# Kernel optimization log

Hardware: AMD Instinct MI355X
Metric: run time of the kernel (lower is better)

## Reference

```python
import jax, jax.numpy as jnp
import numpy as np

B, S, D = 8, 2048, 512

def setup_inputs() -> dict:
    key = jax.random.key(0)
    k1, k2, k3 = jax.random.split(key, 3)
    context = jax.random.normal(k1, (B, S, D), dtype=jnp.float32)
    # nn.Linear default init ~ U(-1/sqrt(D), 1/sqrt(D)); scale keeps softmax sane
    bound = 1.0 / np.sqrt(D)
    W_in = jax.random.uniform(k2, (D, D), dtype=jnp.float32, minval=-bound, maxval=bound)
    W_out = jax.random.uniform(k3, (D, D), dtype=jnp.float32, minval=-bound, maxval=bound)
    return {"context": context, "W_in": W_in, "W_out": W_out}

def reference(context, W_in, W_out):
    # linear_in: x @ W_in.T (torch Linear convention)
    c = jnp.einsum('bsd,ed->bse', context, W_in)            # [B,S,D]
    scores = jnp.einsum('bsd,btd->bst', c, c)               # [B,S,S], no 1/sqrt(d) scale
    attn = jax.nn.softmax(scores, axis=-1)                  # [B,S,S]
    ctx = jnp.einsum('bst,btd->bsd', attn, c)               # [B,S,D]
    out = jnp.einsum('bsd,ed->bse', jnp.tanh(ctx), W_out)   # linear_out
    return out, attn
```

## Files before the change

### kernel.cpp

```cpp
#include <hip/hip_runtime.h>
#include <cstdint>
#include <cstddef>

#define Bc 8
#define Sc 2048
#define Dc 512

typedef float f32x4 __attribute__((ext_vector_type(4)));
typedef __bf16 bf16x8 __attribute__((ext_vector_type(8)));

__device__ __forceinline__ void gload_lds16(const void* g, void* l) {
    __builtin_amdgcn_global_load_lds((const __attribute__((address_space(1))) void*)g,
                                     (__attribute__((address_space(3))) void*)l, 16, 0, 0);
}

__device__ __forceinline__ f32x4 mfma16x16x32(bf16x8 a, bf16x8 b, f32x4 c) {
    return __builtin_amdgcn_mfma_f32_16x16x32_bf16(a, b, c, 0, 0, 0);
}

__global__ void k_convert_w(const float* __restrict__ wi, const float* __restrict__ wo,
                            __bf16* __restrict__ wib, __bf16* __restrict__ wob) {
    int i = blockIdx.x * 256 + threadIdx.x;
    wib[i] = (__bf16)wi[i];
    wob[i] = (__bf16)wo[i];
}

template <bool STATS>
__global__ __launch_bounds__(256) void k_gemm_bf16(
        const __bf16* __restrict__ A, const __bf16* __restrict__ Bt,
        float* __restrict__ C, float2* __restrict__ stats,
        int lda, int ldb, int ldc, int K,
        size_t aOffZ, size_t bOffZ, size_t cOffZ)
{
    __shared__ alignas(16) __bf16 smem[2 * 128 * 64];
    __bf16* As = smem;
    __bf16* Bs = smem + 128 * 64;
    const int tid  = threadIdx.x;
    const int wave = tid >> 6, lane = tid & 63;
    const int waveM = wave >> 1, waveN = wave & 1;
    const int row0 = blockIdx.y * 128;
    const int col0 = blockIdx.x * 128;
    A  += (size_t)blockIdx.z * aOffZ;
    Bt += (size_t)blockIdx.z * bOffZ;
    C  += (size_t)blockIdx.z * cOffZ;

    f32x4 acc[4][4] = {};

    for (int k0 = 0; k0 < K; k0 += 64) {
        #pragma unroll
        for (int i = 0; i < 4; ++i) {
            int flat = i * 2048 + wave * 512 + lane * 8;
            int r  = flat >> 6;
            int cc = (flat >> 3) & 7;
            int gc = (cc ^ (r & 7)) << 3;
            gload_lds16(A  + (size_t)(row0 + r) * lda + k0 + gc, As + i * 2048 + wave * 512);
            gload_lds16(Bt + (size_t)(col0 + r) * ldb + k0 + gc, Bs + i * 2048 + wave * 512);
        }
        __syncthreads();
        #pragma unroll
        for (int ks = 0; ks < 2; ++ks) {
            const int kc = ks * 4 + (lane >> 4);
            bf16x8 av[4], bv[4];
            #pragma unroll
            for (int mi = 0; mi < 4; ++mi) {
                int r = waveM * 64 + mi * 16 + (lane & 15);
                av[mi] = *(const bf16x8*)&As[r * 64 + ((kc ^ (r & 7)) << 3)];
            }
            #pragma unroll
            for (int ni = 0; ni < 4; ++ni) {
                int r = waveN * 64 + ni * 16 + (lane & 15);
                bv[ni] = *(const bf16x8*)&Bs[r * 64 + ((kc ^ (r & 7)) << 3)];
            }
            #pragma unroll
            for (int mi = 0; mi < 4; ++mi)
                #pragma unroll
                for (int ni = 0; ni < 4; ++ni)
                    acc[mi][ni] = mfma16x16x32(av[mi], bv[ni], acc[mi][ni]);
        }
        __syncthreads();
    }

    const int rb = (lane >> 4) << 2;
    const int cb = lane & 15;
    #pragma unroll
    for (int mi = 0; mi < 4; ++mi)
        #pragma unroll
        for (int ni = 0; ni < 4; ++ni) {
            int gr = row0 + waveM * 64 + mi * 16 + rb;
            int gc = col0 + waveN * 64 + ni * 16 + cb;
            #pragma unroll
            for (int rr = 0; rr < 4; ++rr)
                C[(size_t)(gr + rr) * ldc + gc] = acc[mi][ni][rr];
        }

    if constexpr (STATS) {
        float2* sm = (float2*)smem;
        #pragma unroll
        for (int mi = 0; mi < 4; ++mi)
            #pragma unroll
            for (int rr = 0; rr < 4; ++rr) {
                float mx = fmaxf(fmaxf(acc[mi][0][rr], acc[mi][1][rr]),
                                 fmaxf(acc[mi][2][rr], acc[mi][3][rr]));
                #pragma unroll
                for (int off = 1; off < 16; off <<= 1) mx = fmaxf(mx, __shfl_xor(mx, off));
                float zs = 0.f;
                #pragma unroll
                for (int ni = 0; ni < 4; ++ni) zs += __expf(acc[mi][ni][rr] - mx);
                #pragma unroll
                for (int off = 1; off < 16; off <<= 1) zs += __shfl_xor(zs, off);
                if ((lane & 15) == 0)
                    sm[waveN * 128 + waveM * 64 + mi * 16 + rb + rr] = make_float2(mx, zs);
            }
        __syncthreads();
        if (tid < 128) {
            float2 a2 = sm[tid], b2 = sm[128 + tid];
            float M = fmaxf(a2.x, b2.x);
            float Z = a2.y * __expf(a2.x - M) + b2.y * __expf(b2.x - M);
            stats[((size_t)blockIdx.z * Sc + row0 + tid) * 16 + blockIdx.x] = make_float2(M, Z);
        }
    }
}

__global__ __launch_bounds__(256) void k_stat_combine(const float2* __restrict__ stats,
                                                      float2* __restrict__ rowstat) {
    int r = blockIdx.x * 256 + threadIdx.x;
    float2 s[16];
    #pragma unroll
    for (int i = 0; i < 16; ++i) s[i] = stats[(size_t)r * 16 + i];
    float M = s[0].x;
    #pragma unroll
    for (int i = 1; i < 16; ++i) M = fmaxf(M, s[i].x);
    float Z = 0.f;
    #pragma unroll
    for (int i = 0; i < 16; ++i) Z += s[i].y * __expf(s[i].x - M);
    rowstat[r] = make_float2(M, 1.f / Z);
}

__global__ __launch_bounds__(512) void k_pv_fused(
        float* __restrict__ attn,
        const __bf16* __restrict__ cT,
        const float2* __restrict__ rowstat,
        __bf16* __restrict__ ctx)
{
    __shared__ alignas(16) __bf16 As[64 * 64];
    __shared__ alignas(16) __bf16 Bs[512 * 64];
    const int tid  = threadIdx.x;
    const int wave = tid >> 6, lane = tid & 63;
    const int b    = blockIdx.y;
    const int row0 = blockIdx.x * 64;
    float* sc = attn + (size_t)b * Sc * Sc;
    const __bf16* Bt = cT + (size_t)b * Dc * Sc;

    const int ar = tid >> 3;
    const int ac = (tid & 7) * 8;
    const float2 st = rowstat[b * Sc + row0 + ar];
    const float m_row = st.x, zinv = st.y;
    const int c8a  = ac >> 3;
    const int aoff = ar * 64 + ((c8a ^ (ar & 7)) << 3);

    f32x4 acc[4][4] = {};

    f32x4 s0 = *(const f32x4*)&sc[(size_t)(row0 + ar) * Sc + ac];
    f32x4 s1 = *(const f32x4*)&sc[(size_t)(row0 + ar) * Sc + ac + 4];

    for (int kt = 0; kt < Sc; kt += 64) {
        #pragma unroll
        for (int i = 0; i < 8; ++i) {
            int chunk = i * 512 + wave * 64 + lane;
            int r  = chunk >> 3;
            int cc = chunk & 7;
            gload_lds16(Bt + (size_t)r * Sc + kt + ((cc ^ (r & 7)) << 3),
                        Bs + (size_t)(i * 512 + wave * 64) * 8);
        }
        f32x4 p0, p1;
        #pragma unroll
        for (int j = 0; j < 4; ++j) {
            p0[j] = __expf(s0[j] - m_row) * zinv;
            p1[j] = __expf(s1[j] - m_row) * zinv;
        }
        *(f32x4*)&sc[(size_t)(row0 + ar) * Sc + kt + ac]     = p0;
        *(f32x4*)&sc[(size_t)(row0 + ar) * Sc + kt + ac + 4] = p1;
        bf16x8 pb;
        #pragma unroll
        for (int j = 0; j < 4; ++j) { pb[j] = (__bf16)p0[j]; pb[4 + j] = (__bf16)p1[j]; }
        *(bf16x8*)&As[aoff] = pb;
        __syncthreads();
        if (kt + 64 < Sc) {
            s0 = *(const f32x4*)&sc[(size_t)(row0 + ar) * Sc + kt + 64 + ac];
            s1 = *(const f32x4*)&sc[(size_t)(row0 + ar) * Sc + kt + 64 + ac + 4];
        }
        #pragma unroll
        for (int ks = 0; ks < 2; ++ks) {
            const int kc = ks * 4 + (lane >> 4);
            bf16x8 av[4], bv[4];
            #pragma unroll
            for (int mi = 0; mi < 4; ++mi) {
                int r = mi * 16 + (lane & 15);
                av[mi] = *(const bf16x8*)&As[r * 64 + ((kc ^ (r & 7)) << 3)];
            }
            #pragma unroll
            for (int ni = 0; ni < 4; ++ni) {
                int r = wave * 64 + ni * 16 + (lane & 15);
                bv[ni] = *(const bf16x8*)&Bs[r * 64 + ((kc ^ (r & 7)) << 3)];
            }
            #pragma unroll
            for (int mi = 0; mi < 4; ++mi)
                #pragma unroll
                for (int ni = 0; ni < 4; ++ni)
                    acc[mi][ni] = mfma16x16x32(av[mi], bv[ni], acc[mi][ni]);
        }
        __syncthreads();
    }

    const int rb = (lane >> 4) << 2;
    const int cb = lane & 15;
    #pragma unroll
    for (int mi = 0; mi < 4; ++mi)
        #pragma unroll
        for (int ni = 0; ni < 4; ++ni) {
            int gr = row0 + mi * 16 + rb;
            int gc = wave * 64 + ni * 16 + cb;
            #pragma unroll
            for (int rr = 0; rr < 4; ++rr)
                ctx[(size_t)(b * Sc + gr + rr) * Dc + gc] = (__bf16)tanhf(acc[mi][ni][rr]);
        }
}

__global__ __launch_bounds__(256) void k_cproj(
        const float* __restrict__ A, const __bf16* __restrict__ Bt,
        __bf16* __restrict__ Cb, __bf16* __restrict__ CTb)
{
    __shared__ alignas(16) char smem[49152];
    float*  Asf = (float*)smem;
    __bf16* Bs  = (__bf16*)(smem + 32768);
    const int tid  = threadIdx.x;
    const int wave = tid >> 6, lane = tid & 63;
    const int waveM = wave >> 1, waveN = wave & 1;
    const int row0 = blockIdx.y * 128;
    const int col0 = blockIdx.x * 128;

    f32x4 acc[4][4] = {};

    for (int k0 = 0; k0 < Dc; k0 += 64) {
        #pragma unroll
        for (int i = 0; i < 8; ++i) {
            int flat = i * 1024 + wave * 256 + lane * 4;
            int r  = flat >> 6;
            int cc = (flat >> 2) & 15;
            int gc = (cc ^ (r & 15)) << 2;
            gload_lds16(A + (size_t)(row0 + r) * Dc + k0 + gc, Asf + i * 1024 + wave * 256);
        }
        #pragma unroll
        for (int i = 0; i < 4; ++i) {
            int flat = i * 2048 + wave * 512 + lane * 8;
            int r  = flat >> 6;
            int cc = (flat >> 3) & 7;
            int gc = (cc ^ (r & 7)) << 3;
            gload_lds16(Bt + (size_t)(col0 + r) * Dc + k0 + gc, Bs + i * 2048 + wave * 512);
        }
        __syncthreads();
        #pragma unroll
        for (int ks = 0; ks < 2; ++ks) {
            const int kc8 = ks * 4 + (lane >> 4);
            const int kc4 = kc8 << 1;
            bf16x8 av[4], bv[4];
            #pragma unroll
            for (int mi = 0; mi < 4; ++mi) {
                int r  = waveM * 64 + mi * 16 + (lane & 15);
                int r4 = r & 15;
                f32x4 lo = *(const f32x4*)&Asf[r * 64 + (((kc4    ) ^ r4) << 2)];
                f32x4 hi = *(const f32x4*)&Asf[r * 64 + (((kc4 + 1) ^ r4) << 2)];
                bf16x8 a;
                a[0] = (__bf16)lo[0]; a[1] = (__bf16)lo[1]; a[2] = (__bf16)lo[2]; a[3] = (__bf16)lo[3];
                a[4] = (__bf16)hi[0]; a[5] = (__bf16)hi[1]; a[6] = (__bf16)hi[2]; a[7] = (__bf16)hi[3];
                av[mi] = a;
            }
            #pragma unroll
            for (int ni = 0; ni < 4; ++ni) {
                int r = waveN * 64 + ni * 16 + (lane & 15);
                bv[ni] = *(const bf16x8*)&Bs[r * 64 + ((kc8 ^ (r & 7)) << 3)];
            }
            #pragma unroll
            for (int mi = 0; mi < 4; ++mi)
                #pragma unroll
                for (int ni = 0; ni < 4; ++ni)
                    acc[mi][ni] = mfma16x16x32(av[mi], bv[ni], acc[mi][ni]);
        }
        __syncthreads();
    }

    const int rb = (lane >> 4) << 2;
    const int cb = lane & 15;
    __bf16* T = (__bf16*)smem;
    #pragma unroll
    for (int mi = 0; mi < 4; ++mi)
        #pragma unroll
        for (int ni = 0; ni < 4; ++ni) {
            int lr = waveM * 64 + mi * 16 + rb;
            int lc = waveN * 64 + ni * 16 + cb;
            #pragma unroll
            for (int rr = 0; rr < 4; ++rr) {
                __bf16 h = (__bf16)acc[mi][ni][rr];
                Cb[(size_t)(row0 + lr + rr) * Dc + col0 + lc] = h;
                T[lc * 136 + lr + rr] = h;
            }
        }
    __syncthreads();
    const int bb = row0 >> 11;
    const int s0 = row0 & 2047;
    #pragma unroll
    for (int i = 0; i < 8; ++i) {
        int n  = i * 16 + (tid >> 4);
        int mo = (tid & 15) * 8;
        bf16x8 v = *(const bf16x8*)&T[n * 136 + mo];
        *(bf16x8*)&CTb[(size_t)bb * Dc * Sc + (size_t)(col0 + n) * Sc + s0 + mo] = v;
    }
}

extern "C" void kernel_launch(void* const* d_in, const int* in_sizes, int n_in,
                              void* d_out, int out_size, void* d_ws, size_t ws_size,
                              hipStream_t stream)
{
    (void)in_sizes; (void)n_in; (void)out_size; (void)ws_size;
    const float* context = (const float*)d_in[0];
    const float* W_in    = (const float*)d_in[1];
    const float* W_out   = (const float*)d_in[2];
    float* out  = (float*)d_out;
    float* attn = out + (size_t)Bc * Sc * Dc;

    char* ws = (char*)d_ws;
    __bf16* c_bf    = (__bf16*)ws;
    __bf16* cT_bf   = (__bf16*)(ws + 16777216);
    __bf16* wi_bf   = (__bf16*)(ws + 33554432);
    __bf16* wo_bf   = (__bf16*)(ws + 34078720);
    float2* stats   = (float2*)(ws + 34603008);
    float2* rowstat = (float2*)(ws + 36700160);

    k_convert_w<<<dim3(Dc * Dc / 256), 256, 0, stream>>>(W_in, W_out, wi_bf, wo_bf);

    k_cproj<<<dim3(Dc / 128, (Bc * Sc) / 128), 256, 0, stream>>>(context, wi_bf, c_bf, cT_bf);

    k_gemm_bf16<true><<<dim3(Sc / 128, Sc / 128, Bc), 256, 0, stream>>>(
        c_bf, c_bf, attn, stats, Dc, Dc, Sc, Dc,
        (size_t)Sc * Dc, (size_t)Sc * Dc, (size_t)Sc * Sc);

    k_stat_combine<<<dim3(Bc * Sc / 256), 256, 0, stream>>>(stats, rowstat);

    k_pv_fused<<<dim3(Sc / 64, Bc), 512, 0, stream>>>(attn, cT_bf, rowstat, c_bf);

    k_gemm_bf16<false><<<dim3(Dc / 128, (Bc * Sc) / 128, 1), 256, 0, stream>>>(
        c_bf, wo_bf, out, nullptr, Dc, Dc, Dc, Dc, 0, 0, 0);
}
```

Before: 203.1 us.

## Halve PV row tile and remap block indices for batch-interleaved scheduling

Result: faster. 191.5 us (-5.7%).

```diff
diff --git a/kernel.cpp b/kernel.cpp
--- a/kernel.cpp
+++ b/kernel.cpp
@@ -8,6 +8,7 @@
 
 typedef float f32x4 __attribute__((ext_vector_type(4)));
 typedef __bf16 bf16x8 __attribute__((ext_vector_type(8)));
+typedef __bf16 bf16x4 __attribute__((ext_vector_type(4)));
 
 __device__ __forceinline__ void gload_lds16(const void* g, void* l) {
     __builtin_amdgcn_global_load_lds((const __attribute__((address_space(1))) void*)g,
@@ -38,11 +39,18 @@
     const int tid  = threadIdx.x;
     const int wave = tid >> 6, lane = tid & 63;
     const int waveM = wave >> 1, waveN = wave & 1;
-    const int row0 = blockIdx.y * 128;
-    const int col0 = blockIdx.x * 128;
-    A  += (size_t)blockIdx.z * aOffZ;
-    Bt += (size_t)blockIdx.z * bOffZ;
-    C  += (size_t)blockIdx.z * cOffZ;
+    int row0, col0, bz;
+    if constexpr (STATS) {
+        const int bid = blockIdx.x;
+        bz   = bid & 7;
+        col0 = ((bid >> 3) & 15) * 128;
+        row0 = (bid >> 7) * 128;
+    } else {
+        bz = blockIdx.z; row0 = blockIdx.y * 128; col0 = blockIdx.x * 128;
+    }
+    A  += (size_t)bz * aOffZ;
+    Bt += (size_t)bz * bOffZ;
+    C  += (size_t)bz * cOffZ;
 
     f32x4 acc[4][4] = {};
 
@@ -116,7 +124,7 @@
             float2 a2 = sm[tid], b2 = sm[128 + tid];
             float M = fmaxf(a2.x, b2.x);
             float Z = a2.y * __expf(a2.x - M) + b2.y * __expf(b2.x - M);
-            stats[((size_t)blockIdx.z * Sc + row0 + tid) * 16 + blockIdx.x] = make_float2(M, Z);
+            stats[((size_t)bz * Sc + row0 + tid) * 16 + (col0 >> 7)] = make_float2(M, Z);
         }
     }
 }
@@ -136,32 +144,31 @@
     rowstat[r] = make_float2(M, 1.f / Z);
 }
 
-__global__ __launch_bounds__(512) void k_pv_fused(
+__global__ __launch_bounds__(512, 4) void k_pv_fused(
         float* __restrict__ attn,
         const __bf16* __restrict__ cT,
         const float2* __restrict__ rowstat,
         __bf16* __restrict__ ctx)
 {
-    __shared__ alignas(16) __bf16 As[64 * 64];
+    __shared__ alignas(16) __bf16 As[32 * 64];
     __shared__ alignas(16) __bf16 Bs[512 * 64];
     const int tid  = threadIdx.x;
     const int wave = tid >> 6, lane = tid & 63;
-    const int b    = blockIdx.y;
-    const int row0 = blockIdx.x * 64;
+    const int b    = blockIdx.x & 7;
+    const int row0 = (blockIdx.x >> 3) * 32;
     float* sc = attn + (size_t)b * Sc * Sc;
     const __bf16* Bt = cT + (size_t)b * Dc * Sc;
 
-    const int ar = tid >> 3;
-    const int ac = (tid & 7) * 8;
+    const int ar = tid >> 4;
+    const int ac = (tid & 15) * 4;
     const float2 st = rowstat[b * Sc + row0 + ar];
     const float m_row = st.x, zinv = st.y;
     const int c8a  = ac >> 3;
-    const int aoff = ar * 64 + ((c8a ^ (ar & 7)) << 3);
-
-    f32x4 acc[4][4] = {};
-
-    f32x4 s0 = *(const f32x4*)&sc[(size_t)(row0 + ar) * Sc + ac];
-    f32x4 s1 = *(const f32x4*)&sc[(size_t)(row0 + ar) * Sc + ac + 4];
+    const int aoff = ar * 64 + ((c8a ^ (ar & 7)) << 3) + (ac & 4);
+
+    f32x4 acc[2][4] = {};
+
+    f32x4 s = *(const f32x4*)&sc[(size_t)(row0 + ar) * Sc + ac];
 
     for (int kt = 0; kt < Sc; kt += 64) {
         #pragma unroll
@@ -172,29 +179,23 @@
             gload_lds16(Bt + (size_t)r * Sc + kt + ((cc ^ (r & 7)) << 3),
                         Bs + (size_t)(i * 512 + wave * 64) * 8);
         }
-        f32x4 p0, p1;
-        #pragma unroll
-        for (int j = 0; j < 4; ++j) {
-            p0[j] = __expf(s0[j] - m_row) * zinv;
-            p1[j] = __expf(s1[j] - m_row) * zinv;
-        }
-        *(f32x4*)&sc[(size_t)(row0 + ar) * Sc + kt + ac]     = p0;
-        *(f32x4*)&sc[(size_t)(row0 + ar) * Sc + kt + ac + 4] = p1;
-        bf16x8 pb;
-        #pragma unroll
-        for (int j = 0; j < 4; ++j) { pb[j] = (__bf16)p0[j]; pb[4 + j] = (__bf16)p1[j]; }
-        *(bf16x8*)&As[aoff] = pb;
-        __syncthreads();
-        if (kt + 64 < Sc) {
-            s0 = *(const f32x4*)&sc[(size_t)(row0 + ar) * Sc + kt + 64 + ac];
-            s1 = *(const f32x4*)&sc[(size_t)(row0 + ar) * Sc + kt + 64 + ac + 4];
-        }
+        f32x4 p;
+        #pragma unroll
+        for (int j = 0; j < 4; ++j) p[j] = __expf(s[j] - m_row) * zinv;
+        bf16x4 pb;
+        #pragma unroll
+        for (int j = 0; j < 4; ++j) pb[j] = (__bf16)p[j];
+        *(bf16x4*)&As[aoff] = pb;
+        __syncthreads();
+        *(f32x4*)&sc[(size_t)(row0 + ar) * Sc + kt + ac] = p;
+        if (kt + 64 < Sc)
+            s = *(const f32x4*)&sc[(size_t)(row0 + ar) * Sc + kt + 64 + ac];
         #pragma unroll
         for (int ks = 0; ks < 2; ++ks) {
             const int kc = ks * 4 + (lane >> 4);
-            bf16x8 av[4], bv[4];
-            #pragma unroll
-            for (int mi = 0; mi < 4; ++mi) {
+            bf16x8 av[2], bv[4];
+            #pragma unroll
+            for (int mi = 0; mi < 2; ++mi) {
                 int r = mi * 16 + (lane & 15);
                 av[mi] = *(const bf16x8*)&As[r * 64 + ((kc ^ (r & 7)) << 3)];
             }
@@ -204,7 +205,7 @@
                 bv[ni] = *(const bf16x8*)&Bs[r * 64 + ((kc ^ (r & 7)) << 3)];
             }
             #pragma unroll
-            for (int mi = 0; mi < 4; ++mi)
+            for (int mi = 0; mi < 2; ++mi)
                 #pragma unroll
                 for (int ni = 0; ni < 4; ++ni)
                     acc[mi][ni] = mfma16x16x32(av[mi], bv[ni], acc[mi][ni]);
@@ -215,7 +216,7 @@
     const int rb = (lane >> 4) << 2;
     const int cb = lane & 15;
     #pragma unroll
-    for (int mi = 0; mi < 4; ++mi)
+    for (int mi = 0; mi < 2; ++mi)
         #pragma unroll
         for (int ni = 0; ni < 4; ++ni) {
             int gr = row0 + mi * 16 + rb;
@@ -340,13 +341,13 @@
 
     k_cproj<<<dim3(Dc / 128, (Bc * Sc) / 128), 256, 0, stream>>>(context, wi_bf, c_bf, cT_bf);
 
-    k_gemm_bf16<true><<<dim3(Sc / 128, Sc / 128, Bc), 256, 0, stream>>>(
+    k_gemm_bf16<true><<<dim3(Bc * 16 * 16), 256, 0, stream>>>(
         c_bf, c_bf, attn, stats, Dc, Dc, Sc, Dc,
         (size_t)Sc * Dc, (size_t)Sc * Dc, (size_t)Sc * Sc);
 
     k_stat_combine<<<dim3(Bc * Sc / 256), 256, 0, stream>>>(stats, rowstat);
 
-    k_pv_fused<<<dim3(Sc / 64, Bc), 512, 0, stream>>>(attn, cT_bf, rowstat, c_bf);
+    k_pv_fused<<<dim3((Sc / 32) * Bc), 512, 0, stream>>>(attn, cT_bf, rowstat, c_bf);
 
     k_gemm_bf16<false><<<dim3(Dc / 128, (Bc * Sc) / 128, 1), 256, 0, stream>>>(
         c_bf, wo_bf, out, nullptr, Dc, Dc, Dc, Dc, 0, 0, 0);
```
